# Kernel optimization log

Measured on AMD Instinct MI355X. Metric: run time of the kernel, lower is better.

Reference implementation:

```python
import jax, jax.numpy as jnp
import numpy as np

NUM_HEADS = 16
ROPE_BASE = 10000.0
EPS = 1e-6


def _rms_norm(x, scale):
    # RMSNorm over last dim with learnable scale (QKNorm over full `dim`).
    var = jnp.mean(jnp.square(x), axis=-1, keepdims=True)
    return x * jax.lax.rsqrt(var + EPS) * scale


def _rotate_half(x):
    x1, x2 = jnp.split(x, 2, axis=-1)
    return jnp.concatenate([-x2, x1], axis=-1)


def _apply_rope(q, k, rotary_dim):
    # q, k: (b, n, h, d); rotate first rotary_dim channels of each head.
    n = q.shape[1]
    half = rotary_dim // 2
    inv_freq = 1.0 / (ROPE_BASE ** (jnp.arange(0, half, dtype=jnp.float32) * 2.0 / rotary_dim))
    freqs = jnp.arange(n, dtype=jnp.float32)[:, None] * inv_freq[None, :]  # (n, half)
    emb = jnp.concatenate([freqs, freqs], axis=-1)  # (n, rotary_dim)
    cos = jnp.cos(emb)[None, :, None, :]
    sin = jnp.sin(emb)[None, :, None, :]

    def rot(x):
        x_rot, x_pass = x[..., :rotary_dim], x[..., rotary_dim:]
        x_rot = x_rot * cos + _rotate_half(x_rot) * sin
        return jnp.concatenate([x_rot, x_pass], axis=-1)

    return rot(q), rot(k)


def setup_inputs() -> dict:
    key = jax.random.key(0)
    ks = jax.random.split(key, 7)
    input_dim, dim = 1024, 1024
    b, n = 2, 2048
    s_in = 1.0 / np.sqrt(input_dim)
    s_d = 1.0 / np.sqrt(dim)
    return {
        "input": jax.random.normal(ks[0], (b, n, input_dim), dtype=jnp.float32),
        "w_qkv": jax.random.normal(ks[1], (input_dim, 3 * dim), dtype=jnp.float32) * s_in,
        "b_qkv": jax.random.normal(ks[2], (3 * dim,), dtype=jnp.float32) * 0.01,
        "q_scale": jnp.ones((dim,), dtype=jnp.float32) + 0.01 * jax.random.normal(ks[3], (dim,)),
        "k_scale": jnp.ones((dim,), dtype=jnp.float32) + 0.01 * jax.random.normal(ks[4], (dim,)),
        "w_out": jax.random.normal(ks[5], (dim, input_dim), dtype=jnp.float32) * s_d,
        "b_out": jax.random.normal(ks[6], (input_dim,), dtype=jnp.float32) * 0.01,
    }


def reference(input, w_qkv, b_qkv, q_scale, k_scale, w_out, b_out):
    b, n, _ = input.shape
    h = NUM_HEADS
    qkv = input @ w_qkv + b_qkv  # (b, n, 3*dim)
    q, k, v = jnp.split(qkv, 3, axis=-1)
    q = _rms_norm(q, q_scale)
    k = _rms_norm(k, k_scale)
    d = q.shape[-1] // h
    q = q.reshape(b, n, h, d)
    k = k.reshape(b, n, h, d)
    v = v.reshape(b, n, h, d)
    q, k = _apply_rope(q, k, rotary_dim=d)  # partial_rotary_factor=1
    scale = d ** (-0.5)
    attn = jnp.einsum("bqhd,bkhd->bhqk", q, k) * scale
    attn = jax.nn.softmax(attn, axis=-1)
    out = jnp.einsum("bhqk,bkhd->bqhd", attn, v).reshape(b, n, h * d)
    return out @ w_out + b_out
```

## Files before the change

### kernel.cpp

```cpp
#include <hip/hip_runtime.h>
#include <stdint.h>

typedef short bf16x8 __attribute__((ext_vector_type(8)));
typedef float f32x4 __attribute__((ext_vector_type(4)));
typedef unsigned short u16;

#define MFMA_BF16 __builtin_amdgcn_mfma_f32_16x16x32_bf16
#define LOG2E 1.44269504088896f

static __device__ __forceinline__ u16 f2bf(float x) {
  union { float f; unsigned u; } v; v.f = x;
  unsigned r = v.u + 0x7fffu + ((v.u >> 16) & 1u);
  return (u16)(r >> 16);
}
static __device__ __forceinline__ float bf2f(u16 h) {
  union { unsigned u; float f; } v; v.u = ((unsigned)h) << 16; return v.f;
}
static __device__ __forceinline__ unsigned cvt_pk_bf16(float lo, float hi) {
  unsigned r;
  asm("v_cvt_pk_bf16_f32 %0, %1, %2" : "=v"(r) : "v"(lo), "v"(hi));
  return r;
}
static __device__ __forceinline__ void gld_lds16(const u16* g, u16* l) {
  __builtin_amdgcn_global_load_lds(
      (const __attribute__((address_space(1))) void*)g,
      (__attribute__((address_space(3))) void*)l, 16, 0, 0);
}

__global__ __launch_bounds__(256) void k_cast(const float* __restrict__ x,
                                              u16* __restrict__ y) {
  int i = blockIdx.x * 256 + threadIdx.x;
  const float4* p = (const float4*)x;
  float4 a = p[i * 2], b = p[i * 2 + 1];
  ushort4 o0, o1;
  o0.x = f2bf(a.x); o0.y = f2bf(a.y); o0.z = f2bf(a.z); o0.w = f2bf(a.w);
  o1.x = f2bf(b.x); o1.y = f2bf(b.y); o1.z = f2bf(b.z); o1.w = f2bf(b.w);
  ushort4* q = (ushort4*)y;
  q[i * 2] = o0; q[i * 2 + 1] = o1;
}

__global__ __launch_bounds__(256) void k_wtrans(const float* __restrict__ w,
                                                u16* __restrict__ wt,
                                                int K, int N) {
  int n = blockIdx.x * 256 + threadIdx.x;
  int k0 = blockIdx.y * 8;
  if (n >= N) return;
  u16 o[8];
#pragma unroll
  for (int j = 0; j < 8; j++) o[j] = f2bf(w[(size_t)(k0 + j) * N + n]);
  *(uint4*)&wt[(size_t)n * K + k0] = *(const uint4*)o;
}

template <int OUT_BF16>
__global__ __launch_bounds__(256, 2) void k_gemm(const u16* __restrict__ A,
                                                 const u16* __restrict__ Bt,
                                                 const float* __restrict__ bias,
                                                 void* __restrict__ Cp,
                                                 int M, int N, int K) {
  __shared__ u16 As[128 * 64];
  __shared__ u16 Bs[128 * 64];
  const int tid = threadIdx.x;
  const int lane = tid & 63;
  const int wid = tid >> 6;
  const int wm = wid >> 1, wn = wid & 1;
  const int m0 = blockIdx.x * 128, n0 = blockIdx.y * 128;

  const int sr = tid >> 3;
  const int sc = tid & 7;
  const int scsw = sc ^ (sr & 7);
  const u16* ga = A + (size_t)(m0 + sr) * K + (scsw << 3);
  const u16* gb = Bt + (size_t)(n0 + sr) * K + (scsw << 3);

  const int ar = wm * 64 + (lane & 15);
  const int br = wn * 64 + (lane & 15);
  const int cs0 = lane >> 4;

  f32x4 acc[4][4] = {};

  for (int k0 = 0; k0 < K; k0 += 64) {
    __syncthreads();
#pragma unroll
    for (int i = 0; i < 4; i++)
      gld_lds16(ga + k0 + i * (32 * K), &As[((tid & ~63) + 256 * i) * 8]);
#pragma unroll
    for (int i = 0; i < 4; i++)
      gld_lds16(gb + k0 + i * (32 * K), &Bs[((tid & ~63) + 256 * i) * 8]);
    __syncthreads();
#pragma unroll
    for (int kk = 0; kk < 2; kk++) {
      bf16x8 af[4], bfr[4];
#pragma unroll
      for (int mi = 0; mi < 4; mi++)
        af[mi] = *(const bf16x8*)&As[(ar + mi * 16) * 64 +
                                     (((kk * 4 + cs0) ^ (ar & 7)) << 3)];
#pragma unroll
      for (int ni = 0; ni < 4; ni++)
        bfr[ni] = *(const bf16x8*)&Bs[(br + ni * 16) * 64 +
                                      (((kk * 4 + cs0) ^ (br & 7)) << 3)];
#pragma unroll
      for (int mi = 0; mi < 4; mi++)
#pragma unroll
        for (int ni = 0; ni < 4; ni++)
          acc[mi][ni] = MFMA_BF16(af[mi], bfr[ni], acc[mi][ni], 0, 0, 0);
    }
  }

  const int crow0 = m0 + wm * 64 + ((lane >> 4) << 2);
  const int ccol0 = n0 + wn * 64 + (lane & 15);
#pragma unroll
  for (int ni = 0; ni < 4; ni++) {
    float bv = bias[ccol0 + ni * 16];
#pragma unroll
    for (int mi = 0; mi < 4; mi++) {
#pragma unroll
      for (int r = 0; r < 4; r++) {
        float v = acc[mi][ni][r] + bv;
        size_t idx = (size_t)(crow0 + mi * 16 + r) * N + ccol0 + ni * 16;
        if (OUT_BF16) ((u16*)Cp)[idx] = f2bf(v);
        else ((float*)Cp)[idx] = v;
      }
    }
  }
}

__global__ __launch_bounds__(256) void k_normrope(const u16* __restrict__ qkv,
                                                  const float* __restrict__ qscale,
                                                  const float* __restrict__ kscale,
                                                  u16* __restrict__ Qb,
                                                  u16* __restrict__ Kb) {
  const int row = blockIdx.x;
  const int b = row >> 11, n = row & 2047;
  const int t = threadIdx.x;
  __shared__ float qn[1024], kn[1024];
  __shared__ float csb[32], snb[32];
  __shared__ float redq[4], redk[4];

  ushort4 q4 = *(const ushort4*)&qkv[(size_t)row * 3072 + t * 4];
  ushort4 k4 = *(const ushort4*)&qkv[(size_t)row * 3072 + 1024 + t * 4];
  float qv[4] = {bf2f(q4.x), bf2f(q4.y), bf2f(q4.z), bf2f(q4.w)};
  float kv[4] = {bf2f(k4.x), bf2f(k4.y), bf2f(k4.z), bf2f(k4.w)};
  float sq = 0.f, sk = 0.f;
#pragma unroll
  for (int j = 0; j < 4; j++) { sq += qv[j] * qv[j]; sk += kv[j] * kv[j]; }
#pragma unroll
  for (int o = 1; o < 64; o <<= 1) {
    sq += __shfl_xor(sq, o);
    sk += __shfl_xor(sk, o);
  }
  if ((t & 63) == 0) { redq[t >> 6] = sq; redk[t >> 6] = sk; }
  if (t < 32) {
    float inv = exp2f(-(float)t * (13.287712379549449f / 32.f));
    float fr = (float)n * inv;
    float s, c;
    sincosf(fr, &s, &c);
    csb[t] = c; snb[t] = s;
  }
  __syncthreads();
  float rq = rsqrtf((redq[0] + redq[1] + redq[2] + redq[3]) * (1.f / 1024.f) + 1e-6f);
  float rk = rsqrtf((redk[0] + redk[1] + redk[2] + redk[3]) * (1.f / 1024.f) + 1e-6f);
#pragma unroll
  for (int j = 0; j < 4; j++) {
    int jj = t * 4 + j;
    qn[jj] = qv[j] * rq * qscale[jj];
    kn[jj] = kv[j] * rk * kscale[jj];
  }
  __syncthreads();
  const int j0 = t * 4;
  const int h = j0 >> 6;
  const int d0 = j0 & 63;
  u16 qo[4], ko[4];
#pragma unroll
  for (int j = 0; j < 4; j++) {
    int jj = j0 + j;
    int dd = d0 + j;
    float c = csb[dd & 31], s = snb[dd & 31];
    float oq, ok;
    if (dd < 32) {
      oq = qn[jj] * c - qn[jj + 32] * s;
      ok = kn[jj] * c - kn[jj + 32] * s;
    } else {
      oq = qn[jj] * c + qn[jj - 32] * s;
      ok = kn[jj] * c + kn[jj - 32] * s;
    }
    qo[j] = f2bf(oq * (0.125f * LOG2E));
    ko[j] = f2bf(ok);
  }
  const size_t base = ((size_t)(b * 16 + h) * 2048 + n) * 64 + d0;
  *(ushort4*)&Qb[base] = *(const ushort4*)qo;
  *(ushort4*)&Kb[base] = *(const ushort4*)ko;
}

__global__ __launch_bounds__(256) void k_vtrans(const u16* __restrict__ qkv,
                                                u16* __restrict__ Vt) {
  const int bh = blockIdx.y;
  const int b = bh >> 4, h = bh & 15;
  const int n0 = blockIdx.x * 64;
  const int t = threadIdx.x;
  __shared__ u16 tile[64][72];
#pragma unroll
  for (int i = 0; i < 2; i++) {
    int r = (t >> 3) + 32 * i;
    int c = t & 7;
    uint4 v = *(const uint4*)&qkv[((size_t)(b * 2048 + n0 + r)) * 3072 + 2048 + h * 64 + c * 8];
    *(uint4*)&tile[r][c * 8] = v;
  }
  __syncthreads();
#pragma unroll
  for (int i = 0; i < 2; i++) {
    int dr = (t >> 3) + 32 * i;
    int c = t & 7;
    u16 vals[8];
#pragma unroll
    for (int j = 0; j < 8; j++) vals[j] = tile[c * 8 + j][dr];
    *(uint4*)&Vt[((size_t)bh * 64 + dr) * 2048 + n0 + c * 8] = *(const uint4*)vals;
  }
}

__global__ __launch_bounds__(512, 4) void k_attn(const u16* __restrict__ Qb,
                                                 const u16* __restrict__ Kb,
                                                 const u16* __restrict__ Vt,
                                                 u16* __restrict__ Ob) {
  const int bh = blockIdx.y;
  const int q0 = blockIdx.x * 128;
  const int t = threadIdx.x, lane = t & 63, wid = t >> 6;
  __shared__ u16 Ks[2][64 * 64];
  __shared__ u16 Vs[2][64 * 64];
  __shared__ u16 Ps[8][16 * 72];
  const u16* Qg = Qb + (size_t)bh * 2048 * 64;
  const u16* Kg = Kb + (size_t)bh * 2048 * 64;
  const u16* Vg = Vt + (size_t)bh * 64 * 2048;

  const int q = lane & 15;
  const int g = lane >> 4;

  bf16x8 qf[2];
#pragma unroll
  for (int kk = 0; kk < 2; kk++)
    qf[kk] = *(const bf16x8*)&Qg[(size_t)(q0 + wid * 16 + q) * 64 +
                                 kk * 32 + (g << 3)];

  f32x4 ot[4] = {};
  float lsum = 0.f;

  const int sr = t >> 3;
  const int sc = t & 7;
  const int scsw = sc ^ (sr & 7);
  const u16* gk = Kg + sr * 64 + (scsw << 3);
  const u16* gv = Vg + (size_t)sr * 2048 + (scsw << 3);
  u16* ldst_k0 = &Ks[0][(t & ~63) * 8];
  u16* ldst_k1 = &Ks[1][(t & ~63) * 8];
  u16* ldst_v0 = &Vs[0][(t & ~63) * 8];
  u16* ldst_v1 = &Vs[1][(t & ~63) * 8];

  gld_lds16(gk, ldst_k0);
  gld_lds16(gv, ldst_v0);
  gld_lds16(gk + (size_t)64 * 64, ldst_k1);
  gld_lds16(gv + 64, ldst_v1);

  u16* pr = &Ps[wid][q * 72];

  for (int it = 0; it < 32; ++it) {
    const int cur = it & 1;
    if (it < 31) asm volatile("s_waitcnt vmcnt(2)" ::: "memory");
    else         asm volatile("s_waitcnt vmcnt(0)" ::: "memory");
    asm volatile("s_barrier" ::: "memory");

    const u16* Kc = Ks[cur];
    const u16* Vc = Vs[cur];

    f32x4 s[4] = {};
#pragma unroll
    for (int kk = 0; kk < 2; kk++) {
      bf16x8 kf[4];
#pragma unroll
      for (int nj = 0; nj < 4; nj++) {
        int kr = nj * 16 + q;
        kf[nj] = *(const bf16x8*)&Kc[kr * 64 + (((kk * 4 + g) ^ (kr & 7)) << 3)];
      }
      __builtin_amdgcn_s_setprio(1);
#pragma unroll
      for (int nj = 0; nj < 4; nj++)
        s[nj] = MFMA_BF16(kf[nj], qf[kk], s[nj], 0, 0, 0);
      __builtin_amdgcn_s_setprio(0);
    }

#pragma unroll
    for (int nj = 0; nj < 4; nj++) {
      float p0 = exp2f(s[nj][0]);
      float p1 = exp2f(s[nj][1]);
      float p2 = exp2f(s[nj][2]);
      float p3 = exp2f(s[nj][3]);
      lsum += (p0 + p1) + (p2 + p3);
      uint2 w;
      w.x = cvt_pk_bf16(p0, p1);
      w.y = cvt_pk_bf16(p2, p3);
      *(uint2*)&pr[nj * 16 + g * 4] = w;
    }

#pragma unroll
    for (int ks = 0; ks < 2; ks++) {
      bf16x8 pb = *(const bf16x8*)&pr[ks * 32 + g * 8];
      bf16x8 vb[4];
#pragma unroll
      for (int dj = 0; dj < 4; dj++) {
        int vr = dj * 16 + q;
        vb[dj] = *(const bf16x8*)&Vc[vr * 64 + (((ks * 4 + g) ^ (vr & 7)) << 3)];
      }
      __builtin_amdgcn_s_setprio(1);
#pragma unroll
      for (int dj = 0; dj < 4; dj++)
        ot[dj] = MFMA_BF16(vb[dj], pb, ot[dj], 0, 0, 0);
      __builtin_amdgcn_s_setprio(0);
    }

    asm volatile("s_barrier" ::: "memory");
    if (it < 30) {
      const int kv2 = (it + 2) * 64;
      gld_lds16(gk + (size_t)kv2 * 64, cur ? ldst_k1 : ldst_k0);
      gld_lds16(gv + kv2, cur ? ldst_v1 : ldst_v0);
    }
  }

  lsum += __shfl_xor(lsum, 16);
  lsum += __shfl_xor(lsum, 32);
  const float invl = 1.f / lsum;

  const int b = bh >> 4, h = bh & 15;
  const int rowq = q0 + wid * 16 + q;
#pragma unroll
  for (int dj = 0; dj < 4; dj++) {
    u16 ov[4];
#pragma unroll
    for (int r = 0; r < 4; r++) ov[r] = f2bf(ot[dj][r] * invl);
    *(ushort4*)&Ob[(size_t)(b * 2048 + rowq) * 1024 + h * 64 + dj * 16 + g * 4] =
        *(const ushort4*)ov;
  }
}

extern "C" void kernel_launch(void* const* d_in, const int* in_sizes, int n_in,
                              void* d_out, int out_size, void* d_ws, size_t ws_size,
                              hipStream_t stream) {
  const float* input = (const float*)d_in[0];
  const float* w_qkv = (const float*)d_in[1];
  const float* b_qkv = (const float*)d_in[2];
  const float* q_scale = (const float*)d_in[3];
  const float* k_scale = (const float*)d_in[4];
  const float* w_out = (const float*)d_in[5];
  const float* b_out = (const float*)d_in[6];
  float* out = (float*)d_out;

  char* ws = (char*)d_ws;
  u16* Abuf  = (u16*)(ws);
  u16* WqkvT = (u16*)(ws + 8388608);
  u16* WoutT = (u16*)(ws + 14680064);
  u16* qkv   = (u16*)(ws + 16777216);
  u16* Qb    = (u16*)(ws + 41943040);
  u16* Kb    = (u16*)(ws + 50331648);
  u16* Vt    = (u16*)(ws + 58720256);
  u16* Attn  = (u16*)(ws + 67108864);

  k_cast<<<2048, 256, 0, stream>>>(input, Abuf);
  k_wtrans<<<dim3(12, 128), 256, 0, stream>>>(w_qkv, WqkvT, 1024, 3072);
  k_wtrans<<<dim3(4, 128), 256, 0, stream>>>(w_out, WoutT, 1024, 1024);
  k_gemm<1><<<dim3(32, 24), 256, 0, stream>>>(Abuf, WqkvT, b_qkv, qkv, 4096, 3072, 1024);
  k_normrope<<<4096, 256, 0, stream>>>(qkv, q_scale, k_scale, Qb, Kb);
  k_vtrans<<<dim3(32, 32), 256, 0, stream>>>(qkv, Vt);
  k_attn<<<dim3(16, 32), 512, 0, stream>>>(Qb, Kb, Vt, Attn);
  k_gemm<0><<<dim3(32, 8), 256, 0, stream>>>(Attn, WoutT, b_out, out, 4096, 1024, 1024);
}
```

Measured before the change: 140.5 us.

## Use 32x32 MFMA with split-KV wave groups and register-resident P in attention

Rewrites the attention kernel to use 32x32x16 MFMA tiles, with each wave owning 32 query rows. The eight waves are split into two groups that process alternating KV tiles through a 4-deep LDS ring, and the partial outputs and sums are merged through shared memory at the end. P now stays in registers and is reshaped with cross-lane shuffles instead of a round trip through LDS. This aims to cut LDS traffic and per-tile barrier overhead, at the cost of more registers, a larger shared-memory footprint (64KB, which may reduce occupancy), and a final reduction step.

Result: no change. 141.4 us (+0.6%).

```diff
diff --git a/kernel.cpp b/kernel.cpp
--- a/kernel.cpp
+++ b/kernel.cpp
@@ -3,9 +3,11 @@
 
 typedef short bf16x8 __attribute__((ext_vector_type(8)));
 typedef float f32x4 __attribute__((ext_vector_type(4)));
+typedef float f32x16 __attribute__((ext_vector_type(16)));
 typedef unsigned short u16;
 
 #define MFMA_BF16 __builtin_amdgcn_mfma_f32_16x16x32_bf16
+#define MFMA32 __builtin_amdgcn_mfma_f32_32x32x16_bf16
 #define LOG2E 1.44269504088896f
 
 static __device__ __forceinline__ u16 f2bf(float x) {
@@ -223,117 +225,133 @@
   const int bh = blockIdx.y;
   const int q0 = blockIdx.x * 128;
   const int t = threadIdx.x, lane = t & 63, wid = t >> 6;
-  __shared__ u16 Ks[2][64 * 64];
-  __shared__ u16 Vs[2][64 * 64];
-  __shared__ u16 Ps[8][16 * 72];
+  const int grp = wid >> 2, sub = wid & 3;
+  const int q = lane & 31, hi = lane >> 5;
+
+  __shared__ u16 smem[32768];
+  u16* Ks = smem;
+  u16* Vs = smem + 4 * 4096;
+
   const u16* Qg = Qb + (size_t)bh * 2048 * 64;
   const u16* Kg = Kb + (size_t)bh * 2048 * 64;
   const u16* Vg = Vt + (size_t)bh * 64 * 2048;
 
-  const int q = lane & 15;
-  const int g = lane >> 4;
-
-  bf16x8 qf[2];
-#pragma unroll
-  for (int kk = 0; kk < 2; kk++)
-    qf[kk] = *(const bf16x8*)&Qg[(size_t)(q0 + wid * 16 + q) * 64 +
-                                 kk * 32 + (g << 3)];
-
-  f32x4 ot[4] = {};
+  bf16x8 qf[4];
+  {
+    const u16* qrow = Qg + (size_t)(q0 + sub * 32 + q) * 64;
+#pragma unroll
+    for (int kk = 0; kk < 4; kk++)
+      qf[kk] = *(const bf16x8*)&qrow[kk * 16 + hi * 8];
+  }
+
+  f32x16 ot[2] = {};
   float lsum = 0.f;
 
-  const int sr = t >> 3;
-  const int sc = t & 7;
-  const int scsw = sc ^ (sr & 7);
-  const u16* gk = Kg + sr * 64 + (scsw << 3);
-  const u16* gv = Vg + (size_t)sr * 2048 + (scsw << 3);
-  u16* ldst_k0 = &Ks[0][(t & ~63) * 8];
-  u16* ldst_k1 = &Ks[1][(t & ~63) * 8];
-  u16* ldst_v0 = &Vs[0][(t & ~63) * 8];
-  u16* ldst_v1 = &Vs[1][(t & ~63) * 8];
-
-  gld_lds16(gk, ldst_k0);
-  gld_lds16(gv, ldst_v0);
-  gld_lds16(gk + (size_t)64 * 64, ldst_k1);
-  gld_lds16(gv + 64, ldst_v1);
-
-  u16* pr = &Ps[wid][q * 72];
-
-  for (int it = 0; it < 32; ++it) {
-    const int cur = it & 1;
-    if (it < 31) asm volatile("s_waitcnt vmcnt(2)" ::: "memory");
-    else         asm volatile("s_waitcnt vmcnt(0)" ::: "memory");
+  const int srow = t >> 3;
+  const int sslot = (t & 7) ^ (srow & 7);
+  const u16* gk = Kg + srow * 64 + (sslot << 3);
+  const u16* gv = Vg + (size_t)srow * 2048 + (sslot << 3);
+  const int ldoff = (t & ~63) * 8;
+
+#define STAGE(tile)                                                     \
+  do {                                                                  \
+    gld_lds16(gk + (size_t)(tile) * 4096, &Ks[((tile) & 3) * 4096 + ldoff]); \
+    gld_lds16(gv + (size_t)(tile) * 64,   &Vs[((tile) & 3) * 4096 + ldoff]); \
+  } while (0)
+
+  STAGE(0); STAGE(1); STAGE(2); STAGE(3);
+
+  for (int s = 0; s < 16; ++s) {
+    if (s < 15) asm volatile("s_waitcnt vmcnt(4)" ::: "memory");
+    else        asm volatile("s_waitcnt vmcnt(0)" ::: "memory");
     asm volatile("s_barrier" ::: "memory");
 
-    const u16* Kc = Ks[cur];
-    const u16* Vc = Vs[cur];
-
-    f32x4 s[4] = {};
-#pragma unroll
-    for (int kk = 0; kk < 2; kk++) {
-      bf16x8 kf[4];
-#pragma unroll
-      for (int nj = 0; nj < 4; nj++) {
-        int kr = nj * 16 + q;
-        kf[nj] = *(const bf16x8*)&Kc[kr * 64 + (((kk * 4 + g) ^ (kr & 7)) << 3)];
-      }
-      __builtin_amdgcn_s_setprio(1);
-#pragma unroll
-      for (int nj = 0; nj < 4; nj++)
-        s[nj] = MFMA_BF16(kf[nj], qf[kk], s[nj], 0, 0, 0);
-      __builtin_amdgcn_s_setprio(0);
-    }
-
-#pragma unroll
-    for (int nj = 0; nj < 4; nj++) {
-      float p0 = exp2f(s[nj][0]);
-      float p1 = exp2f(s[nj][1]);
-      float p2 = exp2f(s[nj][2]);
-      float p3 = exp2f(s[nj][3]);
-      lsum += (p0 + p1) + (p2 + p3);
-      uint2 w;
-      w.x = cvt_pk_bf16(p0, p1);
-      w.y = cvt_pk_bf16(p2, p3);
-      *(uint2*)&pr[nj * 16 + g * 4] = w;
-    }
-
-#pragma unroll
-    for (int ks = 0; ks < 2; ks++) {
-      bf16x8 pb = *(const bf16x8*)&pr[ks * 32 + g * 8];
-      bf16x8 vb[4];
-#pragma unroll
-      for (int dj = 0; dj < 4; dj++) {
-        int vr = dj * 16 + q;
-        vb[dj] = *(const bf16x8*)&Vc[vr * 64 + (((ks * 4 + g) ^ (vr & 7)) << 3)];
-      }
-      __builtin_amdgcn_s_setprio(1);
-#pragma unroll
-      for (int dj = 0; dj < 4; dj++)
-        ot[dj] = MFMA_BF16(vb[dj], pb, ot[dj], 0, 0, 0);
-      __builtin_amdgcn_s_setprio(0);
+    const int myt = 2 * s + grp;
+    const u16* Kc = &Ks[(myt & 3) * 4096];
+    const u16* Vc = &Vs[(myt & 3) * 4096];
+
+    unsigned w[2][8];
+#pragma unroll
+    for (int kvt = 0; kvt < 2; kvt++) {
+      f32x16 sv = {};
+#pragma unroll
+      for (int kk = 0; kk < 4; kk++) {
+        const int kr = kvt * 32 + q;
+        bf16x8 kf = *(const bf16x8*)&Kc[kr * 64 + (((kk * 2 + hi) ^ (kr & 7)) << 3)];
+        __builtin_amdgcn_s_setprio(1);
+        sv = MFMA32(kf, qf[kk], sv, 0, 0, 0);
+        __builtin_amdgcn_s_setprio(0);
+      }
+#pragma unroll
+      for (int i = 0; i < 8; i++) {
+        float p0 = exp2f(sv[2 * i]);
+        float p1 = exp2f(sv[2 * i + 1]);
+        lsum += p0 + p1;
+        w[kvt][i] = cvt_pk_bf16(p0, p1);
+      }
+    }
+
+#pragma unroll
+    for (int ks = 0; ks < 4; ks++) {
+      const int kvt = ks >> 1, i0 = (ks & 1) * 4;
+      unsigned xs0 = hi ? w[kvt][i0 + 0] : w[kvt][i0 + 2];
+      unsigned xs1 = hi ? w[kvt][i0 + 1] : w[kvt][i0 + 3];
+      unsigned y0 = __shfl_xor(xs0, 32);
+      unsigned y1 = __shfl_xor(xs1, 32);
+      union { unsigned u[4]; bf16x8 v; } pf;
+      pf.u[0] = hi ? y0 : w[kvt][i0 + 0];
+      pf.u[1] = hi ? y1 : w[kvt][i0 + 1];
+      pf.u[2] = hi ? w[kvt][i0 + 2] : y0;
+      pf.u[3] = hi ? w[kvt][i0 + 3] : y1;
+#pragma unroll
+      for (int dt = 0; dt < 2; dt++) {
+        const int vr = dt * 32 + q;
+        bf16x8 va = *(const bf16x8*)&Vc[vr * 64 + (((ks * 2 + hi) ^ (vr & 7)) << 3)];
+        __builtin_amdgcn_s_setprio(1);
+        ot[dt] = MFMA32(va, pf.v, ot[dt], 0, 0, 0);
+        __builtin_amdgcn_s_setprio(0);
+      }
     }
 
     asm volatile("s_barrier" ::: "memory");
-    if (it < 30) {
-      const int kv2 = (it + 2) * 64;
-      gld_lds16(gk + (size_t)kv2 * 64, cur ? ldst_k1 : ldst_k0);
-      gld_lds16(gv + kv2, cur ? ldst_v1 : ldst_v0);
-    }
-  }
-
-  lsum += __shfl_xor(lsum, 16);
+    if (s < 14) { STAGE(2 * s + 4); STAGE(2 * s + 5); }
+  }
+#undef STAGE
+
   lsum += __shfl_xor(lsum, 32);
-  const float invl = 1.f / lsum;
-
-  const int b = bh >> 4, h = bh & 15;
-  const int rowq = q0 + wid * 16 + q;
-#pragma unroll
-  for (int dj = 0; dj < 4; dj++) {
-    u16 ov[4];
-#pragma unroll
-    for (int r = 0; r < 4; r++) ov[r] = f2bf(ot[dj][r] * invl);
-    *(ushort4*)&Ob[(size_t)(b * 2048 + rowq) * 1024 + h * 64 + dj * 16 + g * 4] =
-        *(const ushort4*)ov;
+  __syncthreads();
+  float* obuf = (float*)smem;
+  float* lbuf = (float*)(smem + 16384);
+  if (grp == 1) {
+    float* ob = obuf + (sub * 32 + q) * 64;
+#pragma unroll
+    for (int dt = 0; dt < 2; dt++)
+#pragma unroll
+      for (int g = 0; g < 4; g++) {
+        float4 v4 = {ot[dt][4 * g], ot[dt][4 * g + 1], ot[dt][4 * g + 2], ot[dt][4 * g + 3]};
+        *(float4*)&ob[dt * 32 + 8 * g + 4 * hi] = v4;
+      }
+    if (hi == 0) lbuf[sub * 32 + q] = lsum;
+  }
+  __syncthreads();
+  if (grp == 0) {
+    const float* ob = obuf + (sub * 32 + q) * 64;
+    const float invl = 1.f / (lsum + lbuf[sub * 32 + q]);
+    const int b = bh >> 4, h = bh & 15;
+    const int rowq = q0 + sub * 32 + q;
+    u16* orow = Ob + (size_t)(b * 2048 + rowq) * 1024 + h * 64;
+#pragma unroll
+    for (int dt = 0; dt < 2; dt++)
+#pragma unroll
+      for (int g = 0; g < 4; g++) {
+        float4 v4 = *(const float4*)&ob[dt * 32 + 8 * g + 4 * hi];
+        u16 o4[4];
+        o4[0] = f2bf((ot[dt][4 * g + 0] + v4.x) * invl);
+        o4[1] = f2bf((ot[dt][4 * g + 1] + v4.y) * invl);
+        o4[2] = f2bf((ot[dt][4 * g + 2] + v4.z) * invl);
+        o4[3] = f2bf((ot[dt][4 * g + 3] + v4.w) * invl);
+        *(ushort4*)&orow[dt * 32 + 8 * g + 4 * hi] = *(const ushort4*)o4;
+      }
   }
 }
 
```
